# Optimization experiments

Measured on AMD Instinct MI355X. Metric: run time of the kernel, lower is better.

The kernel has to match this reference:

```python
import jax, jax.numpy as jnp
import numpy as np

TOP_N = 10
N_HEADS = 8

def _layernorm(x, g, b, eps=1e-5):
    mu = jnp.mean(x, axis=-1, keepdims=True)
    var = jnp.mean((x - mu) ** 2, axis=-1, keepdims=True)
    return (x - mu) * jax.lax.rsqrt(var + eps) * g + b

def setup_inputs() -> dict:
    key = jax.random.key(0)
    ks = jax.random.split(key, 16)
    B, N, D = 4096, 32768, 512
    s = 1.0 / np.sqrt(D)
    inp = {
        "visit_rep": jax.random.normal(ks[0], (B, D), jnp.float32),
        "E_mem_patient_rep": jax.random.normal(ks[1], (N, D), jnp.float32),
        "E_mem_med_rep": jax.random.normal(ks[2], (N, D), jnp.float32),
        "Wq": jax.random.uniform(ks[3], (D, D), jnp.float32, -s, s),
        "Wk": jax.random.uniform(ks[4], (D, D), jnp.float32, -s, s),
        "Wv": jax.random.uniform(ks[5], (D, D), jnp.float32, -s, s),
        "bq": jnp.zeros((D,), jnp.float32),
        "bk": jnp.zeros((D,), jnp.float32),
        "bv": jnp.zeros((D,), jnp.float32),
        "Wo": jax.random.uniform(ks[6], (D, D), jnp.float32, -s, s),
        "bo": jnp.zeros((D,), jnp.float32),
        "W1": jax.random.uniform(ks[7], (D, D), jnp.float32, -s, s),
        "b1": jax.random.uniform(ks[8], (D,), jnp.float32, -s, s),
        "W2": jax.random.uniform(ks[9], (D, D), jnp.float32, -s, s),
        "b2": jax.random.uniform(ks[10], (D,), jnp.float32, -s, s),
        "ln1_g": jnp.ones((D,), jnp.float32),
        "ln1_b": jnp.zeros((D,), jnp.float32),
        "ln2_g": jnp.ones((D,), jnp.float32),
        "ln2_b": jnp.zeros((D,), jnp.float32),
    }
    return inp

def reference(visit_rep, E_mem_patient_rep, E_mem_med_rep,
              Wq, bq, Wk, bk, Wv, bv, Wo, bo,
              W1, b1, W2, b2, ln1_g, ln1_b, ln2_g, ln2_b):
    B, D = visit_rep.shape
    H = N_HEADS
    hd = D // H
    # --- exact L2 kNN (faiss GpuIndexFlatL2 equivalent), detached ---
    q = jax.lax.stop_gradient(visit_rep)
    M = jax.lax.stop_gradient(E_mem_patient_rep)
    d2 = (jnp.sum(q * q, axis=1, keepdims=True)
          - 2.0 * q @ M.T
          + jnp.sum(M * M, axis=1)[None, :])          # [B, N]
    _, I = jax.lax.top_k(-d2, TOP_N)                    # [B, top_n]
    k = E_mem_patient_rep[I]                            # [B, top_n, D]
    v = E_mem_med_rep[I]                                # [B, top_n, D]
    # --- multihead attention, query seq-len 1 ---
    qh = (visit_rep @ Wq.T + bq).reshape(B, H, hd)
    kh = (k @ Wk.T + bk).reshape(B, TOP_N, H, hd)
    vh = (v @ Wv.T + bv).reshape(B, TOP_N, H, hd)
    scores = jnp.einsum("bhd,bnhd->bhn", qh, kh) / np.sqrt(hd)
    attn = jax.nn.softmax(scores, axis=-1)
    ctx = jnp.einsum("bhn,bnhd->bhd", attn, vh).reshape(B, D)
    attn_out = ctx @ Wo.T + bo
    # --- residual + norms + FFN (dropout = identity in eval) ---
    x = _layernorm(visit_rep + attn_out, ln1_g, ln1_b)
    ff = (jax.nn.leaky_relu(x @ W1.T + b1, 0.01)) @ W2.T + b2
    x = _layernorm(x + ff, ln2_g, ln2_b)
    return x
```

## Files before the change

kernel.cpp:

```cpp
#include <hip/hip_runtime.h>
#include <math.h>

#define BQ 4096
#define NMEM 32768
#define DD 512
#define TOPN 10
#define NBX 128
#define ENT 2048
#define NCF 16
#define LK 6
#define FINF 3.402823466e+38f
#define IMAX 0x7fffffff

typedef __attribute__((ext_vector_type(8))) short    bf16x8;
typedef __attribute__((ext_vector_type(4))) float    f32x4;

__device__ __forceinline__ unsigned short f2bf(float x) {
    unsigned int u = __float_as_uint(x);
    u += 0x7fffu + ((u >> 16) & 1u);
    return (unsigned short)(u >> 16);
}
__device__ __forceinline__ void async_copy16(const void* gp, void* lp) {
    __builtin_amdgcn_global_load_lds(
        (const __attribute__((address_space(1))) void*)gp,
        (__attribute__((address_space(3))) void*)lp, 16, 0, 0);
}
__device__ __forceinline__ bool lt_si(float s, int j, float s2, int j2) {
    return (s < s2) || (s == s2 && j < j2);
}
template<int KN>
__device__ __forceinline__ void topk_insert(float (&ts)[KN], int (&ti)[KN], float s, int j) {
    if (!lt_si(s, j, ts[KN-1], ti[KN-1])) return;
    #pragma unroll
    for (int p = KN-1; p > 0; --p) {
        if (lt_si(s, j, ts[p-1], ti[p-1])) { ts[p] = ts[p-1]; ti[p] = ti[p-1]; }
        else { ts[p] = s; ti[p] = j; return; }
    }
    ts[0] = s; ti[0] = j;
}

struct CastDesc {
    const float* in[7];
    unsigned short* out[7];
    int start[8];
};
__global__ __launch_bounds__(256) void cast_multi_kernel(CastDesc d) {
    int blk = blockIdx.x;
    int seg = 0;
    #pragma unroll
    for (int s = 0; s < 6; ++s) seg += (blk >= d.start[s + 1]) ? 1 : 0;
    int local = blk - d.start[seg];
    int i = (local * 256 + threadIdx.x) * 4;
    float4 v = *(const float4*)(d.in[seg] + i);
    ushort4 o;
    o.x = f2bf(v.x); o.y = f2bf(v.y); o.z = f2bf(v.z); o.w = f2bf(v.w);
    *(ushort4*)(d.out[seg] + i) = o;
}

__global__ __launch_bounds__(256) void cast_norm2_kernel(
        const float* __restrict__ inA, unsigned short* __restrict__ outA,
        const float* __restrict__ inB, unsigned short* __restrict__ outB,
        float* __restrict__ mnorm) {
    const float* in = blockIdx.y ? inB : inA;
    unsigned short* out = blockIdx.y ? outB : outA;
    int row = blockIdx.x * 4 + (threadIdx.x >> 6);
    int lane = threadIdx.x & 63;
    const float* r = in + (size_t)row * DD + lane * 8;
    float4 a = *(const float4*)r;
    float4 b = *(const float4*)(r + 4);
    ushort4 oa, ob;
    oa.x = f2bf(a.x); oa.y = f2bf(a.y); oa.z = f2bf(a.z); oa.w = f2bf(a.w);
    ob.x = f2bf(b.x); ob.y = f2bf(b.y); ob.z = f2bf(b.z); ob.w = f2bf(b.w);
    unsigned short* op = out + (size_t)row * DD + lane * 8;
    *(ushort4*)op = oa; *(ushort4*)(op + 4) = ob;
    if (blockIdx.y == 0) {
        float s = a.x*a.x + a.y*a.y + a.z*a.z + a.w*a.w
                + b.x*b.x + b.y*b.y + b.z*b.z + b.w*b.w;
        #pragma unroll
        for (int off = 32; off; off >>= 1) s += __shfl_xor(s, off, 64);
        if (lane == 0) mnorm[row] = s;
    }
}

__global__ __launch_bounds__(512, 2) void gemm_knn_kernel(
        const unsigned short* __restrict__ Qb,
        const unsigned short* __restrict__ Mb,
        const float* __restrict__ mnorm,
        unsigned* __restrict__ cand_part) {
    __shared__ __align__(16) union {
        struct { unsigned short A[4][256][32]; unsigned short B[4][256][32]; } g;
        unsigned S[64 * 260];
    } sh;
    const int tid  = threadIdx.x;
    const int lane = tid & 63;
    const int wave = tid >> 6;
    const int quad = lane >> 4, c16 = lane & 15;
    const int wm = wave >> 2, wn = wave & 3;
    const int m0 = blockIdx.y * 256, n0 = blockIdx.x * 256;
    const int srow   = tid >> 2;
    const int schunk = (tid & 3) ^ (srow & 3);
    const unsigned short* ag = Qb + (size_t)(m0 + srow) * DD + schunk * 8;
    const unsigned short* bg = Mb + (size_t)(n0 + srow) * DD + schunk * 8;
    const int cq = (quad ^ (c16 & 3)) * 8;

    f32x4  acc[8][4] = {};
    bf16x8 af[2][8], bf[2][4];

#define KSTAGE(tt) do {                                                         \
    const int s_ = (tt) & 3;                                                    \
    async_copy16(ag + (tt)*32,           &sh.g.A[s_][srow][(tid & 3) * 8]);     \
    async_copy16(ag + (tt)*32 + 128*DD,  &sh.g.A[s_][128 + srow][(tid & 3) * 8]);\
    async_copy16(bg + (tt)*32,           &sh.g.B[s_][srow][(tid & 3) * 8]);     \
    async_copy16(bg + (tt)*32 + 128*DD,  &sh.g.B[s_][128 + srow][(tid & 3) * 8]);\
} while (0)

#define KREAD(tt, st) do {                                                      \
    const int s_ = (tt) & 3;                                                    \
    _Pragma("unroll")                                                           \
    for (int mt = 0; mt < 8; ++mt)                                              \
        af[st][mt] = *(const bf16x8*)&sh.g.A[s_][wm*128 + mt*16 + c16][cq];     \
    _Pragma("unroll")                                                           \
    for (int nt = 0; nt < 4; ++nt)                                              \
        bf[st][nt] = *(const bf16x8*)&sh.g.B[s_][wn*64 + nt*16 + c16][cq];      \
} while (0)

#define KMFMA(st) do {                                                          \
    _Pragma("unroll")                                                           \
    for (int mt = 0; mt < 8; ++mt)                                              \
        _Pragma("unroll")                                                       \
        for (int nt = 0; nt < 4; ++nt)                                          \
            acc[mt][nt] = __builtin_amdgcn_mfma_f32_16x16x32_bf16(              \
                af[st][mt], bf[st][nt], acc[mt][nt], 0, 0, 0);                  \
} while (0)

    KSTAGE(0); KSTAGE(1); KSTAGE(2);
    asm volatile("s_waitcnt vmcnt(8)" ::: "memory");
    __builtin_amdgcn_s_barrier();
    __builtin_amdgcn_sched_barrier(0);
    KREAD(0, 0);

    #pragma unroll
    for (int t = 0; t < 16; ++t) {
        if (t < 14)       asm volatile("s_waitcnt vmcnt(4)" ::: "memory");
        else if (t == 14) asm volatile("s_waitcnt vmcnt(0)" ::: "memory");
        if (t < 15) {
            __builtin_amdgcn_s_barrier();
            __builtin_amdgcn_sched_barrier(0);
            KREAD(t + 1, (t + 1) & 1);
        }
        if (t + 3 < 16) KSTAGE(t + 3);
        __builtin_amdgcn_sched_barrier(0);
        __builtin_amdgcn_s_setprio(1);
        KMFMA(t & 1);
        __builtin_amdgcn_s_setprio(0);
    }
#undef KSTAGE
#undef KREAD
#undef KMFMA

    float mn[4];
    #pragma unroll
    for (int nt = 0; nt < 4; ++nt) mn[nt] = mnorm[n0 + wn*64 + nt*16 + c16];
    const int rrow = tid >> 1, rhalf = tid & 1;
    __syncthreads();
    #pragma unroll
    for (int p = 0; p < 4; ++p) {
        if (wn == p) {
            #pragma unroll
            for (int mt = 0; mt < 8; ++mt)
                #pragma unroll
                for (int nt = 0; nt < 4; ++nt) {
                    uint4 w;
                    #pragma unroll
                    for (int r = 0; r < 4; ++r) {
                        float s = fmaxf(fmaf(-2.f, acc[mt][nt][r], mn[nt]), 0.f);
                        (&w.x)[r] = (__float_as_uint(s) & 0xFFFFFF80u)
                                  | (unsigned)((p & 1) * 64 + nt * 16 + c16);
                    }
                    *(uint4*)&sh.S[(nt*16 + c16) * 260 + wm*128 + mt*16 + quad*4] = w;
                }
        }
        __syncthreads();
        unsigned q4[4] = {0xFFFFFFFFu, 0xFFFFFFFFu, 0xFFFFFFFFu, 0xFFFFFFFFu};
        #pragma unroll
        for (int m = 0; m < 32; ++m) {
            unsigned nv = sh.S[(rhalf*32 + m) * 260 + rrow];
            #pragma unroll
            for (int i = 0; i < 4; ++i) {
                unsigned lo = min(q4[i], nv);
                nv = max(q4[i], nv);
                q4[i] = lo;
            }
        }
        unsigned p0 = (unsigned)__shfl_xor((int)q4[0], 1, 64);
        unsigned p1 = (unsigned)__shfl_xor((int)q4[1], 1, 64);
        unsigned p2 = (unsigned)__shfl_xor((int)q4[2], 1, 64);
        unsigned p3 = (unsigned)__shfl_xor((int)q4[3], 1, 64);
        if (rhalf == 0) {
            uint4 w4;
            w4.x = min(q4[0], p3); w4.y = min(q4[1], p2);
            w4.z = min(q4[2], p1); w4.w = min(q4[3], p0);
            *(uint4*)(cand_part + (size_t)(m0 + rrow) * ENT + blockIdx.x * 16 + p * 4) = w4;
        }
        __syncthreads();
    }
}

__global__ __launch_bounds__(256) void knn_select_kernel(
        const unsigned* __restrict__ cand_part,
        const float* __restrict__ Q, const float* __restrict__ Mm,
        const float* __restrict__ mnorm,
        int* __restrict__ knn_idx) {
    const int row = blockIdx.x;
    const int wave = threadIdx.x >> 6, lane = threadIdx.x & 63;
    __shared__ unsigned sk[64];
    __shared__ int      sc[64];
    __shared__ int      ids[NCF];
    __shared__ float    d2s[NCF];

    unsigned ks[LK]; int ti[LK];
    #pragma unroll
    for (int q = 0; q < LK; ++q) { ks[q] = 0xFFFFFFFFu; ti[q] = IMAX; }
    const uint4* p4 = (const uint4*)(cand_part + (size_t)row * ENT) + wave * 128;
    #pragma unroll
    for (int i = 0; i < 2; ++i) {
        uint4 v = p4[lane + 64 * i];
        #pragma unroll
        for (int e = 0; e < 4; ++e) {
            unsigned k = (&v.x)[e];
            int pos = wave * 512 + (lane + 64 * i) * 4 + e;
            int gcol = (pos >> 3) * 128 + (int)(k & 127u);
            bool cm[LK];
            #pragma unroll
            for (int q = 0; q < LK; ++q) cm[q] = k < ks[q];
            #pragma unroll
            for (int q = LK - 1; q > 0; --q) {
                unsigned tns = cm[q] ? k : ks[q];  int tni = cm[q] ? gcol : ti[q];
                ks[q] = cm[q-1] ? ks[q-1] : tns;
                ti[q] = cm[q-1] ? ti[q-1] : tni;
            }
            ks[0] = cm[0] ? k : ks[0];
            ti[0] = cm[0] ? gcol : ti[0];
        }
    }
    #pragma unroll
    for (int r = 0; r < NCF; ++r) {
        unsigned mk = ks[0]; int mi = ti[0];
        #pragma unroll
        for (int off = 1; off < 64; off <<= 1) {
            unsigned ok = (unsigned)__shfl_xor((int)mk, off, 64);
            int      oi = __shfl_xor(mi, off, 64);
            bool t = (ok < mk) || (ok == mk && oi < mi);
            mk = t ? ok : mk; mi = t ? oi : mi;
        }
        bool win = (ks[0] == mk) && (ti[0] == mi);
        #pragma unroll
        for (int q = 0; q < LK - 1; ++q) {
            ks[q] = win ? ks[q+1] : ks[q];
            ti[q] = win ? ti[q+1] : ti[q];
        }
        ks[LK-1] = win ? 0xFFFFFFFFu : ks[LK-1];
        ti[LK-1] = win ? IMAX : ti[LK-1];
        if (lane == r) { sk[wave * NCF + r] = mk; sc[wave * NCF + r] = mi; }
    }
    __syncthreads();
    if (wave == 0) {
        unsigned myk = sk[lane];
        int      myc = sc[lane];
        #pragma unroll
        for (int r = 0; r < NCF; ++r) {
            unsigned mk = myk; int mi = myc;
            #pragma unroll
            for (int off = 1; off < 64; off <<= 1) {
                unsigned ok = (unsigned)__shfl_xor((int)mk, off, 64);
                int      oi = __shfl_xor(mi, off, 64);
                bool t = (ok < mk) || (ok == mk && oi < mi);
                mk = t ? ok : mk; mi = t ? oi : mi;
            }
            bool win = (myk == mk) && (myc == mi);
            myk = win ? 0xFFFFFFFFu : myk;
            myc = win ? IMAX : myc;
            if (lane == r) ids[r] = mi;
        }
    }
    __syncthreads();
    float4 q0 = *(const float4*)(Q + (size_t)row * DD + lane * 8);
    float4 q1 = *(const float4*)(Q + (size_t)row * DD + lane * 8 + 4);
    for (int c = wave; c < NCF; c += 4) {
        int j = ids[c];
        const float* mr = Mm + (size_t)j * DD;
        float4 m0 = *(const float4*)(mr + lane * 8);
        float4 m1 = *(const float4*)(mr + lane * 8 + 4);
        float dot = q0.x*m0.x + q0.y*m0.y + q0.z*m0.z + q0.w*m0.w
                  + q1.x*m1.x + q1.y*m1.y + q1.z*m1.z + q1.w*m1.w;
        #pragma unroll
        for (int off = 32; off; off >>= 1) dot += __shfl_xor(dot, off, 64);
        if (lane == 0) d2s[c] = fmaf(-2.f, dot, mnorm[j]);
    }
    __syncthreads();
    if (threadIdx.x == 0) {
        float ts[TOPN]; int tj[TOPN];
        #pragma unroll
        for (int p = 0; p < TOPN; ++p) { ts[p] = FINF; tj[p] = IMAX; }
        for (int c = 0; c < NCF; ++c) topk_insert<TOPN>(ts, tj, d2s[c], ids[c]);
        #pragma unroll
        for (int p = 0; p < TOPN; ++p) knn_idx[row * TOPN + p] = tj[p];
    }
}

template<int ACT, int OUT_BF16>
__global__ __launch_bounds__(256) void gemm_bf16_nt(
        const unsigned short* __restrict__ A,
        const unsigned short* __restrict__ B,
        const float* __restrict__ bias,
        void* __restrict__ Cout, int ldc) {
    __shared__ __align__(16) unsigned short As[128 * 64];
    __shared__ __align__(16) unsigned short Bs[128 * 64];
    const int tid  = threadIdx.x;
    const int wave = tid >> 6, lane = tid & 63;
    const int quad = lane >> 4, c16 = lane & 15;
    const int m0 = blockIdx.y * 128, n0 = blockIdx.x * 128;
    const int wm0 = (wave >> 1) * 64, wn0 = (wave & 1) * 64;
    const int srow = wave * 32 + (lane >> 3);
    const int schunk = (lane & 7) ^ ((lane >> 3) & 7);
    const int xsw = c16 & 7;

    f32x4 acc[4][4] = {};

    for (int kt = 0; kt < DD; kt += 64) {
        __syncthreads();
        #pragma unroll
        for (int i = 0; i < 4; ++i) {
            const unsigned short* ga = A + (size_t)(m0 + srow + i * 8) * DD + kt + schunk * 8;
            async_copy16(ga, &As[(wave * 32 + i * 8) * 64]);
            const unsigned short* gb = B + (size_t)(n0 + srow + i * 8) * DD + kt + schunk * 8;
            async_copy16(gb, &Bs[(wave * 32 + i * 8) * 64]);
        }
        __syncthreads();
        #pragma unroll
        for (int ks = 0; ks < 64; ks += 32) {
            const int coff = (((ks >> 3) + quad) ^ xsw) << 3;
            bf16x8 af[4], bff[4];
            #pragma unroll
            for (int mt = 0; mt < 4; ++mt)
                af[mt] = *(const bf16x8*)&As[(wm0 + mt * 16 + c16) * 64 + coff];
            #pragma unroll
            for (int nt = 0; nt < 4; ++nt)
                bff[nt] = *(const bf16x8*)&Bs[(wn0 + nt * 16 + c16) * 64 + coff];
            #pragma unroll
            for (int mt = 0; mt < 4; ++mt)
                #pragma unroll
                for (int nt = 0; nt < 4; ++nt)
                    acc[mt][nt] = __builtin_amdgcn_mfma_f32_16x16x32_bf16(
                        af[mt], bff[nt], acc[mt][nt], 0, 0, 0);
        }
    }
    #pragma unroll
    for (int nt = 0; nt < 4; ++nt) {
        int ncol = n0 + wn0 + nt * 16 + c16;
        float bv = bias[ncol];
        #pragma unroll
        for (int mt = 0; mt < 4; ++mt) {
            size_t rbase = (size_t)(m0 + wm0 + mt * 16 + quad * 4) * ldc + ncol;
            #pragma unroll
            for (int r = 0; r < 4; ++r) {
                float v = acc[mt][nt][r] + bv;
                if (ACT == 1) v = v >= 0.f ? v : 0.01f * v;
                if (OUT_BF16) ((unsigned short*)Cout)[rbase + (size_t)r * ldc] = f2bf(v);
                else          ((float*)Cout)[rbase + (size_t)r * ldc] = v;
            }
        }
    }
}

struct G3 {
    const unsigned short* A[3];
    const unsigned short* B[3];
    const float* bias[3];
    void* C[3];
    int obf[3];
};
__global__ __launch_bounds__(256) void gemm3_kernel(G3 g) {
    const int yy = blockIdx.y;
    const int z = (yy >= 512) ? 2 : (yy >= 256 ? 1 : 0);
    const int my = yy - z * 256;
    __shared__ __align__(16) unsigned short As[128 * 64];
    __shared__ __align__(16) unsigned short Bs[128 * 64];
    const unsigned short* A = g.A[z];
    const unsigned short* B = g.B[z];
    const int tid  = threadIdx.x;
    const int wave = tid >> 6, lane = tid & 63;
    const int quad = lane >> 4, c16 = lane & 15;
    const int m0 = my * 128, n0 = blockIdx.x * 128;
    const int wm0 = (wave >> 1) * 64, wn0 = (wave & 1) * 64;
    const int srow = wave * 32 + (lane >> 3);
    const int schunk = (lane & 7) ^ ((lane >> 3) & 7);
    const int xsw = c16 & 7;

    f32x4 acc[4][4] = {};

    for (int kt = 0; kt < DD; kt += 64) {
        __syncthreads();
        #pragma unroll
        for (int i = 0; i < 4; ++i) {
            const unsigned short* ga = A + (size_t)(m0 + srow + i * 8) * DD + kt + schunk * 8;
            async_copy16(ga, &As[(wave * 32 + i * 8) * 64]);
            const unsigned short* gb = B + (size_t)(n0 + srow + i * 8) * DD + kt + schunk * 8;
            async_copy16(gb, &Bs[(wave * 32 + i * 8) * 64]);
        }
        __syncthreads();
        #pragma unroll
        for (int ks = 0; ks < 64; ks += 32) {
            const int coff = (((ks >> 3) + quad) ^ xsw) << 3;
            bf16x8 af[4], bff[4];
            #pragma unroll
            for (int mt = 0; mt < 4; ++mt)
                af[mt] = *(const bf16x8*)&As[(wm0 + mt * 16 + c16) * 64 + coff];
            #pragma unroll
            for (int nt = 0; nt < 4; ++nt)
                bff[nt] = *(const bf16x8*)&Bs[(wn0 + nt * 16 + c16) * 64 + coff];
            #pragma unroll
            for (int mt = 0; mt < 4; ++mt)
                #pragma unroll
                for (int nt = 0; nt < 4; ++nt)
                    acc[mt][nt] = __builtin_amdgcn_mfma_f32_16x16x32_bf16(
                        af[mt], bff[nt], acc[mt][nt], 0, 0, 0);
        }
    }
    const int obf = g.obf[z];
    #pragma unroll
    for (int nt = 0; nt < 4; ++nt) {
        int ncol = n0 + wn0 + nt * 16 + c16;
        float bv = g.bias[z][ncol];
        #pragma unroll
        for (int mt = 0; mt < 4; ++mt) {
            size_t rbase = (size_t)(m0 + wm0 + mt * 16 + quad * 4) * DD + ncol;
            #pragma unroll
            for (int r = 0; r < 4; ++r) {
                float v = acc[mt][nt][r] + bv;
                if (obf) ((unsigned short*)g.C[z])[rbase + (size_t)r * DD] = f2bf(v);
                else     ((float*)g.C[z])[rbase + (size_t)r * DD] = v;
            }
        }
    }
}

__global__ __launch_bounds__(512) void attn_kernel(
        const float* __restrict__ qh, const unsigned short* __restrict__ Kall,
        const unsigned short* __restrict__ Vall, const int* __restrict__ knn_idx,
        unsigned short* __restrict__ ctx_b) {
    const int b = blockIdx.x;
    const int h = threadIdx.x >> 6;
    const int l = threadIdx.x & 63;
    const int col = (h << 6) + l;
    int idxs[TOPN];
    #pragma unroll
    for (int n = 0; n < TOPN; ++n) idxs[n] = knn_idx[b * TOPN + n];
    const float q = qh[(size_t)b * DD + col];
    float sc[TOPN];
    #pragma unroll
    for (int n = 0; n < TOPN; ++n) {
        float p = q * __uint_as_float((unsigned)Kall[(size_t)idxs[n] * DD + col] << 16);
        #pragma unroll
        for (int off = 32; off; off >>= 1) p += __shfl_xor(p, off, 64);
        sc[n] = p * 0.125f;
    }
    float mx = sc[0];
    #pragma unroll
    for (int n = 1; n < TOPN; ++n) mx = fmaxf(mx, sc[n]);
    float se = 0.f;
    #pragma unroll
    for (int n = 0; n < TOPN; ++n) { sc[n] = expf(sc[n] - mx); se += sc[n]; }
    const float inv = 1.f / se;
    float o = 0.f;
    #pragma unroll
    for (int n = 0; n < TOPN; ++n)
        o = fmaf(sc[n] * inv,
                 __uint_as_float((unsigned)Vall[(size_t)idxs[n] * DD + col] << 16), o);
    ctx_b[(size_t)b * DD + col] = f2bf(o);
}

template<int EMIT_BF16>
__global__ __launch_bounds__(256) void add_ln_kernel(
        const float* __restrict__ X, const float* __restrict__ Y,
        const float* __restrict__ g, const float* __restrict__ be,
        float* __restrict__ out, unsigned short* __restrict__ out_b) {
    const int row = blockIdx.x;
    const int t = threadIdx.x;
    const size_t base = (size_t)row * DD;
    float v0 = X[base + t]       + Y[base + t];
    float v1 = X[base + 256 + t] + Y[base + 256 + t];
    float s = v0 + v1, sq = v0 * v0 + v1 * v1;
    #pragma unroll
    for (int off = 32; off; off >>= 1) { s += __shfl_xor(s, off, 64); sq += __shfl_xor(sq, off, 64); }
    __shared__ float rs[4], rq[4];
    const int w = t >> 6, l = t & 63;
    if (l == 0) { rs[w] = s; rq[w] = sq; }
    __syncthreads();
    float tot  = rs[0] + rs[1] + rs[2] + rs[3];
    float totq = rq[0] + rq[1] + rq[2] + rq[3];
    float mu = tot * (1.f / DD);
    float var = totq * (1.f / DD) - mu * mu;
    float rstd = rsqrtf(var + 1e-5f);
    float o0 = (v0 - mu) * rstd * g[t]       + be[t];
    float o1 = (v1 - mu) * rstd * g[256 + t] + be[256 + t];
    out[base + t] = o0;
    out[base + 256 + t] = o1;
    if (EMIT_BF16) {
        out_b[base + t] = f2bf(o0);
        out_b[base + 256 + t] = f2bf(o1);
    }
}

extern "C" void kernel_launch(void* const* d_in, const int* in_sizes, int n_in,
                              void* d_out, int out_size, void* d_ws, size_t ws_size,
                              hipStream_t stream) {
    const float* visit = (const float*)d_in[0];
    const float* Epat  = (const float*)d_in[1];
    const float* Emed  = (const float*)d_in[2];
    const float* Wq = (const float*)d_in[3];
    const float* Wk = (const float*)d_in[4];
    const float* Wv = (const float*)d_in[5];
    const float* bq = (const float*)d_in[6];
    const float* bk = (const float*)d_in[7];
    const float* bv = (const float*)d_in[8];
    const float* Wo = (const float*)d_in[9];
    const float* bo = (const float*)d_in[10];
    const float* W1 = (const float*)d_in[11];
    const float* b1 = (const float*)d_in[12];
    const float* W2 = (const float*)d_in[13];
    const float* b2 = (const float*)d_in[14];
    const float* ln1g = (const float*)d_in[15];
    const float* ln1b = (const float*)d_in[16];
    const float* ln2g = (const float*)d_in[17];
    const float* ln2b = (const float*)d_in[18];
    float* out = (float*)d_out;

    char* base = (char*)d_ws;
    const size_t MB = 1u << 20;
    float* mnorm   = (float*)(base);
    int*   knn_idx = (int*)  (base + 2*MB);
    float* qh      = (float*)(base + 3*MB);
    float* attn_o  = qh;
    float* x1      = (float*)(base + 11*MB);
    float* ff      = (float*)(base + 19*MB);
    unsigned short* Qb    = (unsigned short*)(base + 27*MB);
    unsigned short* ctx_b = (unsigned short*)(base + 31*MB);
    unsigned short* x1_b  = (unsigned short*)(base + 35*MB);
    unsigned short* h1_b  = (unsigned short*)(base + 39*MB);
    unsigned short* Wq_b  = (unsigned short*)(base + 43*MB);
    unsigned short* Wk_b  = Wq_b + 262144;
    unsigned short* Wv_b  = Wk_b + 262144;
    unsigned short* Wo_b  = Wv_b + 262144;
    unsigned short* W1_b  = Wo_b + 262144;
    unsigned short* W2_b  = W1_b + 262144;
    unsigned short* Mb     = (unsigned short*)(base + 46*MB);
    unsigned short* Emed_b = (unsigned short*)(base + 78*MB);
    unsigned short* Kall = (unsigned short*)(base + 110*MB);
    unsigned short* Vall = Kall + (size_t)NMEM * DD;
    unsigned* cand_part = (unsigned*)Kall;

    cast_norm2_kernel<<<dim3(NMEM / 4, 2), 256, 0, stream>>>(Epat, Mb, Emed, Emed_b, mnorm);
    CastDesc cd;
    cd.in[0] = visit; cd.out[0] = Qb;
    cd.in[1] = Wq; cd.in[2] = Wk; cd.in[3] = Wv; cd.in[4] = Wo; cd.in[5] = W1; cd.in[6] = W2;
    cd.out[1] = Wq_b; cd.out[2] = Wk_b; cd.out[3] = Wv_b; cd.out[4] = Wo_b; cd.out[5] = W1_b; cd.out[6] = W2_b;
    cd.start[0] = 0; cd.start[1] = 2048;
    for (int s = 2; s <= 7; ++s) cd.start[s] = cd.start[s-1] + 256;
    cast_multi_kernel<<<cd.start[7], 256, 0, stream>>>(cd);

    gemm_knn_kernel<<<dim3(NBX, BQ / 256), 512, 0, stream>>>(Qb, Mb, mnorm, cand_part);
    knn_select_kernel<<<BQ, 256, 0, stream>>>(cand_part, visit, Epat, mnorm, knn_idx);

    G3 g3;
    g3.A[0] = Mb;     g3.B[0] = Wk_b; g3.bias[0] = bk; g3.C[0] = Kall; g3.obf[0] = 1;
    g3.A[1] = Emed_b; g3.B[1] = Wv_b; g3.bias[1] = bv; g3.C[1] = Vall; g3.obf[1] = 1;
    g3.A[2] = Qb;     g3.B[2] = Wq_b; g3.bias[2] = bq; g3.C[2] = qh;   g3.obf[2] = 0;
    gemm3_kernel<<<dim3(4, 544), 256, 0, stream>>>(g3);

    attn_kernel<<<BQ, 512, 0, stream>>>(qh, Kall, Vall, knn_idx, ctx_b);

    gemm_bf16_nt<0,0><<<dim3(4, BQ / 128), 256, 0, stream>>>(ctx_b, Wo_b, bo, attn_o, DD);
    add_ln_kernel<1><<<BQ, 256, 0, stream>>>(visit, attn_o, ln1g, ln1b, x1, x1_b);
    gemm_bf16_nt<1,1><<<dim3(4, BQ / 128), 256, 0, stream>>>(x1_b, W1_b, b1, h1_b, DD);
    gemm_bf16_nt<0,0><<<dim3(4, BQ / 128), 256, 0, stream>>>(h1_b, W2_b, b2, ff,   DD);
    add_ln_kernel<0><<<BQ, 256, 0, stream>>>(x1, ff, ln2g, ln2b, out, nullptr);
}
```

Baseline: 603.2 us.

## Split GEMM main loop into two half-phases with finer LDS reads and new swizzle

```diff
diff --git a/kernel.cpp b/kernel.cpp
--- a/kernel.cpp
+++ b/kernel.cpp
@@ -98,65 +98,83 @@
     const int wm = wave >> 2, wn = wave & 3;
     const int m0 = blockIdx.y * 256, n0 = blockIdx.x * 256;
     const int srow   = tid >> 2;
-    const int schunk = (tid & 3) ^ (srow & 3);
+    const int schunk = (tid & 3) ^ ((tid >> 3) & 3);
     const unsigned short* ag = Qb + (size_t)(m0 + srow) * DD + schunk * 8;
     const unsigned short* bg = Mb + (size_t)(n0 + srow) * DD + schunk * 8;
-    const int cq = (quad ^ (c16 & 3)) * 8;
+    const int cq = (quad ^ ((c16 >> 1) & 3)) * 8;
 
     f32x4  acc[8][4] = {};
-    bf16x8 af[2][8], bf[2][4];
-
-#define KSTAGE(tt) do {                                                         \
+    bf16x8 af[4], bf[4];
+
+#define STG_A(tt) do {                                                          \
     const int s_ = (tt) & 3;                                                    \
     async_copy16(ag + (tt)*32,           &sh.g.A[s_][srow][(tid & 3) * 8]);     \
     async_copy16(ag + (tt)*32 + 128*DD,  &sh.g.A[s_][128 + srow][(tid & 3) * 8]);\
+} while (0)
+#define STG_B(tt) do {                                                          \
+    const int s_ = (tt) & 3;                                                    \
     async_copy16(bg + (tt)*32,           &sh.g.B[s_][srow][(tid & 3) * 8]);     \
     async_copy16(bg + (tt)*32 + 128*DD,  &sh.g.B[s_][128 + srow][(tid & 3) * 8]);\
 } while (0)
-
-#define KREAD(tt, st) do {                                                      \
+#define RD_A(tt, mh) do {                                                       \
     const int s_ = (tt) & 3;                                                    \
     _Pragma("unroll")                                                           \
-    for (int mt = 0; mt < 8; ++mt)                                              \
-        af[st][mt] = *(const bf16x8*)&sh.g.A[s_][wm*128 + mt*16 + c16][cq];     \
+    for (int mt2 = 0; mt2 < 4; ++mt2)                                           \
+        af[mt2] = *(const bf16x8*)&sh.g.A[s_][wm*128 + ((mh)*4 + mt2)*16 + c16][cq];\
+} while (0)
+#define RD_B(tt) do {                                                           \
+    const int s_ = (tt) & 3;                                                    \
     _Pragma("unroll")                                                           \
     for (int nt = 0; nt < 4; ++nt)                                              \
-        bf[st][nt] = *(const bf16x8*)&sh.g.B[s_][wn*64 + nt*16 + c16][cq];      \
+        bf[nt] = *(const bf16x8*)&sh.g.B[s_][wn*64 + nt*16 + c16][cq];          \
 } while (0)
-
-#define KMFMA(st) do {                                                          \
+#define MM(mh) do {                                                             \
     _Pragma("unroll")                                                           \
-    for (int mt = 0; mt < 8; ++mt)                                              \
+    for (int mt2 = 0; mt2 < 4; ++mt2)                                           \
         _Pragma("unroll")                                                       \
         for (int nt = 0; nt < 4; ++nt)                                          \
-            acc[mt][nt] = __builtin_amdgcn_mfma_f32_16x16x32_bf16(              \
-                af[st][mt], bf[st][nt], acc[mt][nt], 0, 0, 0);                  \
+            acc[(mh)*4 + mt2][nt] = __builtin_amdgcn_mfma_f32_16x16x32_bf16(    \
+                af[mt2], bf[nt], acc[(mh)*4 + mt2][nt], 0, 0, 0);               \
 } while (0)
 
-    KSTAGE(0); KSTAGE(1); KSTAGE(2);
+    STG_A(0); STG_B(0); STG_A(1); STG_B(1); STG_A(2); STG_B(2);
     asm volatile("s_waitcnt vmcnt(8)" ::: "memory");
     __builtin_amdgcn_s_barrier();
     __builtin_amdgcn_sched_barrier(0);
-    KREAD(0, 0);
 
     #pragma unroll
     for (int t = 0; t < 16; ++t) {
-        if (t < 14)       asm volatile("s_waitcnt vmcnt(4)" ::: "memory");
-        else if (t == 14) asm volatile("s_waitcnt vmcnt(0)" ::: "memory");
-        if (t < 15) {
-            __builtin_amdgcn_s_barrier();
-            __builtin_amdgcn_sched_barrier(0);
-            KREAD(t + 1, (t + 1) & 1);
-        }
-        if (t + 3 < 16) KSTAGE(t + 3);
+        RD_A(t, 0); RD_B(t);
+        if (t + 3 < 16) STG_A(t + 3);
+        __builtin_amdgcn_sched_barrier(0);
+        __builtin_amdgcn_s_barrier();
+        asm volatile("s_waitcnt lgkmcnt(0)" ::: "memory");
         __builtin_amdgcn_sched_barrier(0);
         __builtin_amdgcn_s_setprio(1);
-        KMFMA(t & 1);
+        MM(0);
         __builtin_amdgcn_s_setprio(0);
-    }
-#undef KSTAGE
-#undef KREAD
-#undef KMFMA
+        __builtin_amdgcn_sched_barrier(0);
+        __builtin_amdgcn_s_barrier();
+        RD_A(t, 1);
+        if (t + 3 < 16) STG_B(t + 3);
+        if (t <= 12)      asm volatile("s_waitcnt vmcnt(8)" ::: "memory");
+        else if (t == 13) asm volatile("s_waitcnt vmcnt(4)" ::: "memory");
+        else if (t == 14) asm volatile("s_waitcnt vmcnt(0)" ::: "memory");
+        __builtin_amdgcn_sched_barrier(0);
+        __builtin_amdgcn_s_barrier();
+        asm volatile("s_waitcnt lgkmcnt(0)" ::: "memory");
+        __builtin_amdgcn_sched_barrier(0);
+        __builtin_amdgcn_s_setprio(1);
+        MM(1);
+        __builtin_amdgcn_s_setprio(0);
+        __builtin_amdgcn_sched_barrier(0);
+        __builtin_amdgcn_s_barrier();
+    }
+#undef STG_A
+#undef STG_B
+#undef RD_A
+#undef RD_B
+#undef MM
 
     float mn[4];
     #pragma unroll
```

After: 599.0 us. Within noise of the previous version (-0.7%).
